# Optimization experiments

Hardware: AMD Instinct MI355X
Metric: run time of the kernel (lower is better)

## Reference

```python
import jax, jax.numpy as jnp
import numpy as np

# Model dims (match init_kwargs)
B, S, D, H = 2, 1024, 1024, 8
NKV = 1024            # num_key_values = nearest square to 4*D/4 = D -> 32^2
NK = 32               # sqrt(num_key_values) = PK num_keys
NP = 2                # product_keys
DK = D // 16          # PK dim_key
TK = 8                # product_key_topk == final_topk == key_value_pk_topk


def setup_inputs() -> dict:
    key = jax.random.key(0)
    ks = jax.random.split(key, 7)
    std = jnp.float32(0.02)
    return {
        "inputs": jax.random.normal(ks[0], (B, S, D), jnp.float32),
        "Wq": jax.random.normal(ks[1], (D * H, D), jnp.float32) * std,       # to_queries (torch Linear [out,in])
        "Wpk": jax.random.normal(ks[2], (DK * NP * H, D), jnp.float32) * std, # PK.to_queries
        "pk_keys": jax.random.normal(ks[3], (NP, NK, H, DK), jnp.float32) * std,
        "keys_emb": jax.random.normal(ks[4], (NKV * H, D), jnp.float32) * std,
        "values_emb": jax.random.normal(ks[5], (NKV * H, D), jnp.float32) * std,
        "Wo": jax.random.normal(ks[6], (D, D * H), jnp.float32) * std,        # to_out
    }


def reference(inputs, Wq, Wpk, pk_keys, keys_emb, values_emb, Wo):
    b, s, d = inputs.shape
    # queries: per-head dim == d; scale by d**-0.5
    q = (inputs @ Wq.T).reshape(b, s, H, d).transpose(0, 2, 1, 3) * (d ** -0.5)  # [B,H,S,D]

    # ---- PK product-key routing ----
    pq = (inputs @ Wpk.T).reshape(b, s, NP, H, DK)
    sim = jnp.einsum('bsphd,pnhd->pbshn', pq, pk_keys)          # [NP,B,S,H,NK]
    sc, ix = jax.lax.top_k(sim, TK)                             # [NP,B,S,H,TK]
    # combine the two sub-key spaces (strides = [1, NK])
    comb_ix = (ix[0][..., :, None] + ix[1][..., None, :] * NK).reshape(b, s, H, TK * TK)
    comb_sc = (sc[0][..., :, None] + sc[1][..., None, :]).reshape(b, s, H, TK * TK)
    fsc, pki = jax.lax.top_k(comb_sc, TK)                       # final_topk = TK
    fidx = jnp.take_along_axis(comb_ix, pki, axis=-1)           # [B,S,H,TK]
    w = jax.nn.softmax(fsc, axis=-1)                            # softmax_scores=True

    # ---- per-head offset + EmbeddingBag('sum') lookups with per-sample weights ----
    idx = fidx + (jnp.arange(H) * NKV)[None, None, :, None]     # [B,S,H,TK]
    k = jnp.einsum('bshtd,bsht->bhsd', keys_emb[idx], w)        # weighted-sum bag
    v = jnp.einsum('bshtd,bsht->bhsd', values_emb[idx], w)

    # ---- causal attention ----
    att = jnp.einsum('bhqd,bhkd->bhqk', q, k)                   # [B,H,S,S]
    causal = jnp.triu(jnp.ones((s, s), bool), 1)
    att = jnp.where(causal, -jnp.finfo(att.dtype).max, att)
    att = jax.nn.softmax(att, axis=-1)
    out = jnp.einsum('bhqk,bhkd->bqhd', att, v).reshape(b, s, H * d)
    return out @ Wo.T
```

## Files before the change

### kernel.cpp

```cpp
#include <hip/hip_runtime.h>
#include <hip/hip_bf16.h>

#define BB   2
#define SS   1024
#define DD   1024
#define HH   8
#define NPP  2
#define NKK  32
#define DKK  64
#define TKK  8
#define NKV_ 1024

typedef __hip_bfloat16 bf16;
typedef __attribute__((ext_vector_type(8))) short bf16x8;
typedef __attribute__((ext_vector_type(4))) float f32x4;

using u32g = __attribute__((address_space(1))) unsigned int;
using u32l = __attribute__((address_space(3))) unsigned int;

#define GLDS16(g, l) __builtin_amdgcn_global_load_lds((const u32g*)(g), (u32l*)(l), 16, 0, 0)

__device__ inline unsigned short f2b(float f) {
    unsigned x = __float_as_uint(f);
    return (unsigned short)((x + 0x7fffu + ((x >> 16) & 1u)) >> 16);
}
__device__ inline float b2f(unsigned short u) {
    return __uint_as_float(((unsigned)u) << 16);
}

__global__ __launch_bounds__(256) void cvt_bf(const float* __restrict__ src,
                                              bf16* __restrict__ dst, long long n)
{
    long long i = ((long long)blockIdx.x * 256 + threadIdx.x) * 4;
    if (i >= n) return;
    float4 v = *(const float4*)&src[i];
    ushort4 u; u.x = f2b(v.x); u.y = f2b(v.y); u.z = f2b(v.z); u.w = f2b(v.w);
    *(ushort4*)&dst[i] = u;
}

__global__ __launch_bounds__(256) void cvt_bf3(
    const float* __restrict__ s0, bf16* __restrict__ d0, long long n0,
    const float* __restrict__ s1, bf16* __restrict__ d1, long long n1,
    const float* __restrict__ s2, bf16* __restrict__ d2, long long n2)
{
    long long i = ((long long)blockIdx.x * 256 + threadIdx.x) * 4;
    const float* s; bf16* d;
    if (i < n0)                { s = s0 + i;            d = d0 + i; }
    else if (i < n0 + n1)      { s = s1 + (i - n0);     d = d1 + (i - n0); }
    else if (i < n0 + n1 + n2) { s = s2 + (i - n0 - n1); d = d2 + (i - n0 - n1); }
    else return;
    float4 v = *(const float4*)s;
    ushort4 u; u.x = f2b(v.x); u.y = f2b(v.y); u.z = f2b(v.z); u.w = f2b(v.w);
    *(ushort4*)d = u;
}

__global__ __launch_bounds__(256) void reduce_split(
    const float* __restrict__ p, float* __restrict__ out,
    long long n, int nsplit, float scale)
{
    long long i = ((long long)blockIdx.x * 256 + threadIdx.x) * 4;
    if (i >= n) return;
    float4 a = *(const float4*)&p[i];
    for (int s = 1; s < nsplit; ++s) {
        float4 b = *(const float4*)&p[i + (long long)s * n];
        a.x += b.x; a.y += b.y; a.z += b.z; a.w += b.w;
    }
    a.x *= scale; a.y *= scale; a.z *= scale; a.w *= scale;
    *(float4*)&out[i] = a;
}

template<typename TC, int CAUSAL, int GROUP>
__global__ __launch_bounds__(256) void mgemm(
    const bf16* __restrict__ A, const bf16* __restrict__ B, TC* __restrict__ C,
    int K, int lda, int ldb, int ldc,
    long long sAb, long long sAh, long long sBb, long long sBh,
    long long sCb, long long sCh, int zH, float scale)
{
    int gx = gridDim.x, gy = gridDim.y;
    int nwg = gx * gy * gridDim.z;
    int hw  = (blockIdx.z * gy + blockIdx.y) * gx + blockIdx.x;
    int w   = (hw & 7) * (nwg >> 3) + (hw >> 3);
    int z  = w / (gx * gy);
    int r  = w % (gx * gy);
    int bx = (r / (gy * GROUP)) * GROUP + (r % GROUP);
    int by = (r / GROUP) % gy;

    int zb = z / zH, zh = z % zH;
    A += (long long)zb * sAb + (long long)zh * sAh;
    B += (long long)zb * sBb + (long long)zh * sBh;
    C += (long long)zb * sCb + (long long)zh * sCh;

    int row0 = by * 128, col0 = bx * 128;
    if (CAUSAL == 1 && col0 > row0 + 127) return;
    int Klim = (CAUSAL == 2) ? min(K, row0 + 128) : K;

    __shared__ short sh[16384];
    short* As = sh;
    short* Bs = sh + 8192;

    int tid = threadIdx.x, wave = tid >> 6, lane = tid & 63;
    int wr = wave >> 1, wc = wave & 1;
    int lr = lane & 15, lg = lane >> 4;

    f32x4 zero = {0.f, 0.f, 0.f, 0.f};
    f32x4 acc[4][4];
    #pragma unroll
    for (int m = 0; m < 4; ++m)
        #pragma unroll
        for (int n = 0; n < 4; ++n) acc[m][n] = zero;

    int srow = wave * 32 + (lane >> 3);
    int scol = ((lane & 7) ^ (lane >> 3)) * 8;
    int fo = (lg ^ (lr & 7)) * 8;

    for (int k0 = 0; k0 < Klim; k0 += 64) {
        const bf16* Ak = A + (long long)(row0 + srow) * lda + k0 + scol;
        const bf16* Bk = B + (long long)(col0 + srow) * ldb + k0 + scol;
        #pragma unroll
        for (int i = 0; i < 4; ++i) {
            GLDS16(Ak + (long long)i * 8 * lda, &As[(wave * 32 + i * 8) * 64]);
            GLDS16(Bk + (long long)i * 8 * ldb, &Bs[(wave * 32 + i * 8) * 64]);
        }
        asm volatile("s_waitcnt vmcnt(0)" ::: "memory");
        __syncthreads();

        #pragma unroll
        for (int kk = 0; kk < 2; ++kk) {
            bf16x8 af[4], bfr[4];
            #pragma unroll
            for (int m = 0; m < 4; ++m)
                af[m] = *(const bf16x8*)&As[(wr * 64 + m * 16 + lr) * 64 + (fo ^ (kk * 32))];
            #pragma unroll
            for (int n = 0; n < 4; ++n)
                bfr[n] = *(const bf16x8*)&Bs[(wc * 64 + n * 16 + lr) * 64 + (fo ^ (kk * 32))];
            #pragma unroll
            for (int m = 0; m < 4; ++m)
                #pragma unroll
                for (int n = 0; n < 4; ++n)
                    acc[m][n] = __builtin_amdgcn_mfma_f32_16x16x32_bf16(
                        bfr[n], af[m], acc[m][n], 0, 0, 0);
        }
        __syncthreads();
    }

    #pragma unroll
    for (int m = 0; m < 4; ++m) {
        long long row = row0 + wr * 64 + m * 16 + lr;
        #pragma unroll
        for (int n = 0; n < 4; ++n) {
            int col = col0 + wc * 64 + n * 16 + lg * 4;
            if constexpr (sizeof(TC) == 2) {
                ushort4 o;
                o.x = f2b(scale * acc[m][n][0]);
                o.y = f2b(scale * acc[m][n][1]);
                o.z = f2b(scale * acc[m][n][2]);
                o.w = f2b(scale * acc[m][n][3]);
                *(ushort4*)&C[row * ldc + col] = o;
            } else {
                *(float4*)&C[row * ldc + col] = make_float4(
                    scale * acc[m][n][0], scale * acc[m][n][1],
                    scale * acc[m][n][2], scale * acc[m][n][3]);
            }
        }
    }
}

#define TILE 64
#define KT   16
#define LPAD 4
__global__ __launch_bounds__(256) void pq_fix(
    const float* __restrict__ A, const float* __restrict__ Bm, float* __restrict__ P)
{
    long long zo = (long long)blockIdx.z * 1024 * 1024;
    A += zo;
    int col0 = blockIdx.x * TILE;
    int kbase = blockIdx.y * 256;
    __shared__ float As[KT][TILE + LPAD];
    __shared__ float Bs[KT][TILE + LPAD];
    int tid = threadIdx.x, tx = tid % 16, ty = tid / 16;
    float acc[4][4] = {{0.f}};
    int lr = tid / 4, lk = (tid % 4) * 4;

    for (int k0 = kbase; k0 < kbase + 256; k0 += KT) {
        float4 va = *(const float4*)&A[(long long)lr * 1024 + k0 + lk];
        As[lk + 0][lr] = va.x; As[lk + 1][lr] = va.y;
        As[lk + 2][lr] = va.z; As[lk + 3][lr] = va.w;
        float4 vb = *(const float4*)&Bm[(long long)(col0 + lr) * 1024 + k0 + lk];
        Bs[lk + 0][lr] = vb.x; Bs[lk + 1][lr] = vb.y;
        Bs[lk + 2][lr] = vb.z; Bs[lk + 3][lr] = vb.w;
        __syncthreads();
        #pragma unroll
        for (int kk = 0; kk < KT; ++kk) {
            float a[4], b[4];
            #pragma unroll
            for (int i = 0; i < 4; ++i) a[i] = As[kk][ty * 4 + i];
            #pragma unroll
            for (int j = 0; j < 4; ++j) b[j] = Bs[kk][tx * 4 + j];
            #pragma unroll
            for (int i = 0; i < 4; ++i)
                #pragma unroll
                for (int j = 0; j < 4; ++j)
                    acc[i][j] = fmaf(a[i], b[j], acc[i][j]);
        }
        __syncthreads();
    }
    long long base = ((long long)(blockIdx.y * 2 + blockIdx.z) * 64) * 1024;
    #pragma unroll
    for (int i = 0; i < 4; ++i)
        *(float4*)&P[base + (long long)(ty * 4 + i) * 1024 + col0 + tx * 4] =
            make_float4(acc[i][0], acc[i][1], acc[i][2], acc[i][3]);
}

__global__ __launch_bounds__(256) void pq_fix_red(
    const float* __restrict__ P, float* __restrict__ pqb)
{
    long long i4 = ((long long)blockIdx.x * 256 + threadIdx.x) * 4;
    if (i4 >= 131072) return;
    float4 a = *(const float4*)&P[i4];
    #pragma unroll
    for (int sp = 1; sp < 4; ++sp) {
        float4 b = *(const float4*)&P[(long long)sp * 131072 + i4];
        a.x += b.x; a.y += b.y; a.z += b.z; a.w += b.w;
    }
    long long z = i4 >> 16, rem = i4 & 65535;
    *(float4*)&pqb[z * 1048576 + rem] = a;
}

__device__ inline unsigned ord_f32(float f) {
    unsigned u = __float_as_uint(f);
    return (u >> 31) ? ~u : (u | 0x80000000u);
}
__device__ inline float unord_f32(unsigned m) {
    unsigned u = (m >> 31) ? (m ^ 0x80000000u) : ~m;
    return __uint_as_float(u);
}

__global__ __launch_bounds__(256) void pk_route(
    const float* __restrict__ pq, const float* __restrict__ pkk,
    float* __restrict__ wts, int* __restrict__ idxs)
{
    int bid  = blockIdx.x * 4 + (threadIdx.x >> 6);
    int lane = threadIdx.x & 63;
    int h    = bid % HH;
    long long bs = bid / HH;
    int p = lane >> 5, n = lane & 31;

    const float* pv = pq  + (bs * NPP + p) * (HH * DKK) + h * DKK;
    const float* kv = pkk + ((long long)(p * NKK + n) * HH + h) * DKK;
    float s = 0.f;
    #pragma unroll
    for (int d = 0; d < DKK; d += 4) {
        float4 q4 = *(const float4*)&pv[d];
        float4 k4 = *(const float4*)&kv[d];
        s = fmaf(q4.x, k4.x, fmaf(q4.y, k4.y, fmaf(q4.z, k4.z, fmaf(q4.w, k4.w, s))));
    }

    unsigned long long key =
        ((unsigned long long)ord_f32(s) << 32) | (unsigned)(31 - n);
    #pragma unroll
    for (int k = 2; k <= 32; k <<= 1) {
        #pragma unroll
        for (int j = k >> 1; j > 0; j >>= 1) {
            unsigned long long other = __shfl_xor(key, j);
            bool keep_big = ((n & k) == 0) == ((n & j) == 0);
            key = (keep_big == (other > key)) ? other : key;
        }
    }
    float keepv = unord_f32((unsigned)(key >> 32));
    int   keepn = 31 - (int)(key & 31);

    int ci = lane >> 3, cj = lane & 7;
    float c0 = __shfl(keepv, ci);
    float c1 = __shfl(keepv, 32 + cj);
    float cv = c0 + c1;

    unsigned long long k2 =
        ((unsigned long long)ord_f32(cv) << 32) | (unsigned)(63 - lane);
    #pragma unroll
    for (int k = 2; k <= 64; k <<= 1) {
        #pragma unroll
        for (int j = k >> 1; j > 0; j >>= 1) {
            unsigned long long other = __shfl_xor(k2, j);
            bool keep_big = ((lane & k) == 0) == ((lane & j) == 0);
            k2 = (keep_big == (other > k2)) ? other : k2;
        }
    }
    int   f   = 63 - (int)(k2 & 63);
    float fsv = unord_f32((unsigned)(k2 >> 32));
    int n0 = __shfl(keepn, f >> 3);
    int n1 = __shfl(keepn, 32 + (f & 7));
    int fsi = n0 + n1 * NKK;

    float m0 = __shfl(fsv, 0);
    float e = (lane < TKK) ? expf(fsv - m0) : 0.f;
    float sum = e;
    #pragma unroll
    for (int off = 1; off < 8; off <<= 1) sum += __shfl_xor(sum, off);
    if (lane < TKK) {
        wts[(long long)bid * TKK + lane]  = e / sum;
        idxs[(long long)bid * TKK + lane] = fsi + h * NKV_;
    }
}

__global__ __launch_bounds__(256) void gather_kv(
    const bf16* __restrict__ keb, const bf16* __restrict__ veb,
    const float* __restrict__ wts, const int* __restrict__ idxs,
    bf16* __restrict__ kb, bf16* __restrict__ vsd)
{
    int bid = blockIdx.x;
    int h = bid % HH;
    int bs = bid / HH;
    int b = bs / SS, s = bs % SS;

    float w[TKK]; long long rb[TKK];
    #pragma unroll
    for (int t = 0; t < TKK; ++t) {
        w[t]  = wts[(long long)bid * TKK + t];
        rb[t] = (long long)idxs[(long long)bid * TKK + t] * DD;
    }
    int c0 = threadIdx.x * 4;
    long long off = (((long long)b * HH + h) * SS + s) * DD + c0;

    ushort4 ld[TKK];
    #pragma unroll
    for (int t = 0; t < TKK; ++t) ld[t] = *(const ushort4*)&keb[rb[t] + c0];
    float4 a = {0.f, 0.f, 0.f, 0.f};
    #pragma unroll
    for (int t = 0; t < TKK; ++t) {
        a.x += w[t] * b2f(ld[t].x); a.y += w[t] * b2f(ld[t].y);
        a.z += w[t] * b2f(ld[t].z); a.w += w[t] * b2f(ld[t].w);
    }
    ushort4 o; o.x = f2b(a.x); o.y = f2b(a.y); o.z = f2b(a.z); o.w = f2b(a.w);
    *(ushort4*)&kb[off] = o;

    #pragma unroll
    for (int t = 0; t < TKK; ++t) ld[t] = *(const ushort4*)&veb[rb[t] + c0];
    a = make_float4(0.f, 0.f, 0.f, 0.f);
    #pragma unroll
    for (int t = 0; t < TKK; ++t) {
        a.x += w[t] * b2f(ld[t].x); a.y += w[t] * b2f(ld[t].y);
        a.z += w[t] * b2f(ld[t].z); a.w += w[t] * b2f(ld[t].w);
    }
    o.x = f2b(a.x); o.y = f2b(a.y); o.z = f2b(a.z); o.w = f2b(a.w);
    *(ushort4*)&vsd[off] = o;
}

__global__ __launch_bounds__(256) void tr64ip(bf16* __restrict__ m)
{
    __shared__ unsigned short La[64][65];
    __shared__ unsigned short Lb[64][65];
    unsigned short* M = (unsigned short*)m + (long long)blockIdx.y * SS * DD;

    int p = blockIdx.x, ti = 0;
    while (p >= 16 - ti) { p -= 16 - ti; ++ti; }
    int tj = ti + p;
    int a0r = ti * 64, a0c = tj * 64;
    int b0r = tj * 64, b0c = ti * 64;

    int r = threadIdx.x / 16, c4 = (threadIdx.x % 16) * 4;
    #pragma unroll
    for (int i = 0; i < 4; ++i) {
        int sr = r + i * 16;
        ushort4 va = *(const ushort4*)&M[(long long)(a0r + sr) * DD + a0c + c4];
        La[sr][c4] = va.x; La[sr][c4+1] = va.y; La[sr][c4+2] = va.z; La[sr][c4+3] = va.w;
        if (ti != tj) {
            ushort4 vb = *(const ushort4*)&M[(long long)(b0r + sr) * DD + b0c + c4];
            Lb[sr][c4] = vb.x; Lb[sr][c4+1] = vb.y; Lb[sr][c4+2] = vb.z; Lb[sr][c4+3] = vb.w;
        }
    }
    __syncthreads();
    #pragma unroll
    for (int i = 0; i < 4; ++i) {
        int dr = r + i * 16;
        ushort4 va;
        va.x = La[c4][dr]; va.y = La[c4+1][dr]; va.z = La[c4+2][dr]; va.w = La[c4+3][dr];
        *(ushort4*)&M[(long long)(b0r + dr) * DD + b0c + c4] = va;
        if (ti != tj) {
            ushort4 vb;
            vb.x = Lb[c4][dr]; vb.y = Lb[c4+1][dr]; vb.z = Lb[c4+2][dr]; vb.w = Lb[c4+3][dr];
            *(ushort4*)&M[(long long)(a0r + dr) * DD + a0c + c4] = vb;
        }
    }
}

__global__ __launch_bounds__(256) void softmax_rows(bf16* __restrict__ sc)
{
    int r    = blockIdx.x * 4 + (threadIdx.x >> 6);
    int lane = threadIdx.x & 63;
    int sq   = r % SS;
    unsigned short* row = (unsigned short*)(sc + (long long)r * SS);
    int nvalid = sq + 1;
    int wlim = ((sq >> 7) + 1) << 7;
    int base = lane * 16;

    uint4 u0 = *(const uint4*)&row[base];
    uint4 u1 = *(const uint4*)&row[base + 8];
    unsigned uw[8] = {u0.x, u0.y, u0.z, u0.w, u1.x, u1.y, u1.z, u1.w};

    float v[16];
    float m = -INFINITY;
    #pragma unroll
    for (int i = 0; i < 8; ++i) {
        int j0 = base + i * 2;
        v[i*2]   = (j0     < nvalid) ? __uint_as_float(uw[i] << 16)          : -INFINITY;
        v[i*2+1] = (j0 + 1 < nvalid) ? __uint_as_float(uw[i] & 0xffff0000u) : -INFINITY;
        m = fmaxf(m, fmaxf(v[i*2], v[i*2+1]));
    }
    #pragma unroll
    for (int off = 1; off < 64; off <<= 1) m = fmaxf(m, __shfl_xor(m, off));

    float e[16], ls = 0.f;
    #pragma unroll
    for (int i = 0; i < 16; ++i) {
        e[i] = (base + i < nvalid) ? expf(v[i] - m) : 0.f;
        ls += e[i];
    }
    #pragma unroll
    for (int off = 1; off < 64; off <<= 1) ls += __shfl_xor(ls, off);
    float inv = 1.f / ls;

    if (base < wlim) {
        unsigned ow[8];
        #pragma unroll
        for (int i = 0; i < 8; ++i)
            ow[i] = (unsigned)f2b(e[i*2] * inv) | ((unsigned)f2b(e[i*2+1] * inv) << 16);
        *(uint4*)&row[base]     = make_uint4(ow[0], ow[1], ow[2], ow[3]);
        *(uint4*)&row[base + 8] = make_uint4(ow[4], ow[5], ow[6], ow[7]);
    }
}

extern "C" void kernel_launch(void* const* d_in, const int* in_sizes, int n_in,
                              void* d_out, int out_size, void* d_ws, size_t ws_size,
                              hipStream_t stream)
{
    const float* inputs     = (const float*)d_in[0];
    const float* Wq         = (const float*)d_in[1];
    const float* Wpk        = (const float*)d_in[2];
    const float* pk_keys    = (const float*)d_in[3];
    const float* keys_emb   = (const float*)d_in[4];
    const float* values_emb = (const float*)d_in[5];
    const float* Wo         = (const float*)d_in[6];
    float* out = (float*)d_out;

    const long long MB = 1LL << 20;
    char* base = (char*)d_ws;
    bf16* kb  = (bf16*)(base);
    float* spl = (float*)base;
    bf16* qc  = (bf16*)(base + 32*MB);
    bf16* vt  = (bf16*)(base + 64*MB);
    char* screg = base + 96*MB;
    bf16* scb = (bf16*)screg;
    float* pqb = (float*)screg;
    bf16* Wpkb = (bf16*)(screg + 8*MB);
    bf16* Wqb  = (bf16*)(screg + 10*MB);
    bf16* xb   = (bf16*)(screg + 26*MB);
    bf16* keb  = (bf16*)screg;
    bf16* veb  = (bf16*)(screg + 16*MB);
    bf16* Wob  = (bf16*)screg;
    float* wtb = (float*)(base + 128*MB);
    int*   ixb = (int*)(base + 128*MB + (512<<10));
    size_t needed = (size_t)(129*MB);
    if (ws_size < needed) return;

    const long long SLAB = (long long)SS * HH * DD;
    const long long SD   = (long long)SS * DD;
    const long long OUTN = 2048LL * 1024;

    cvt_bf3<<<dim3(11264), 256, 0, stream>>>(
        inputs, xb, 2097152LL, Wpk, Wpkb, 1048576LL, Wq, Wqb, 8388608LL);

    mgemm<float, 0, 1><<<dim3(8, 16, 2), 256, 0, stream>>>(
        xb, Wpkb, spl, 512, 1024, 1024, 1024,
        512, 0, 512, 0, OUTN, 0, 1, 1.0f);
    reduce_split<<<dim3(2048), 256, 0, stream>>>(spl, pqb, OUTN, 2, 1.0f);

    pq_fix<<<dim3(16, 4, 2), 256, 0, stream>>>(inputs, Wpk, spl);
    pq_fix_red<<<dim3(128), 256, 0, stream>>>(spl, pqb);

    pk_route<<<dim3(BB * SS * HH / 4), 256, 0, stream>>>(pqb, pk_keys, wtb, ixb);

    mgemm<bf16, 0, 8><<<dim3(64, 16, 1), 256, 0, stream>>>(
        xb, Wqb, qc, 1024, 1024, 1024, 8192,
        0, 0, 0, 0, 0, 0, 1, 0.03125f);

    cvt_bf3<<<dim3(16384), 256, 0, stream>>>(
        keys_emb, keb, 8388608LL, values_emb, veb, 8388608LL,
        (const float*)nullptr, (bf16*)nullptr, 0LL);

    gather_kv<<<dim3(BB * SS * HH), 256, 0, stream>>>(
        keb, veb, wtb, ixb, kb, vt);

    tr64ip<<<dim3(136, BB * HH), 256, 0, stream>>>(vt);

    mgemm<bf16, 1, 1><<<dim3(8, 8, BB * HH), 256, 0, stream>>>(
        qc, kb, scb, 1024, 8192, 1024, 1024,
        SLAB, (long long)DD, (long long)HH * SD, SD,
        (long long)HH * SS * SS, (long long)SS * SS, HH, 1.0f);

    softmax_rows<<<dim3(BB * HH * SS / 4), 256, 0, stream>>>(scb);

    mgemm<bf16, 2, 1><<<dim3(8, 8, BB * HH), 256, 0, stream>>>(
        scb, vt, qc, 1024, 1024, 1024, 8192,
        (long long)HH * SS * SS, (long long)SS * SS,
        (long long)HH * SD, SD,
        SLAB, (long long)DD, HH, 1.0f);

    cvt_bf<<<dim3(8192), 256, 0, stream>>>(Wo, Wob, 8388608LL);

    mgemm<float, 0, 1><<<dim3(8, 16, 4), 256, 0, stream>>>(
        qc, Wob, spl, 2048, 8192, 8192, 1024,
        2048, 0, 2048, 0, OUTN, 0, 1, 1.0f);
    reduce_split<<<dim3(2048), 256, 0, stream>>>(spl, out, OUTN, 4, 1.0f);
}
```

Before: 356.9 us.

## Pipeline GEMM K-loop with four-stage LDS ring buffer

```diff
diff --git a/kernel.cpp b/kernel.cpp
--- a/kernel.cpp
+++ b/kernel.cpp
@@ -93,10 +93,9 @@
     int row0 = by * 128, col0 = bx * 128;
     if (CAUSAL == 1 && col0 > row0 + 127) return;
     int Klim = (CAUSAL == 2) ? min(K, row0 + 128) : K;
-
-    __shared__ short sh[16384];
-    short* As = sh;
-    short* Bs = sh + 8192;
+    int nt = Klim >> 6;
+
+    __shared__ short sh[4][16384];
 
     int tid = threadIdx.x, wave = tid >> 6, lane = tid & 63;
     int wr = wave >> 1, wc = wave & 1;
@@ -113,17 +112,35 @@
     int scol = ((lane & 7) ^ (lane >> 3)) * 8;
     int fo = (lg ^ (lr & 7)) * 8;
 
-    for (int k0 = 0; k0 < Klim; k0 += 64) {
-        const bf16* Ak = A + (long long)(row0 + srow) * lda + k0 + scol;
-        const bf16* Bk = B + (long long)(col0 + srow) * ldb + k0 + scol;
+    const bf16* Abase = A + (long long)(row0 + srow) * lda + scol;
+    const bf16* Bbase = B + (long long)(col0 + srow) * ldb + scol;
+
+    auto STAGE = [&](int b, int t) {
+        int k0 = t * 64;
+        short* As = &sh[b][0];
+        short* Bs = &sh[b][8192];
         #pragma unroll
         for (int i = 0; i < 4; ++i) {
-            GLDS16(Ak + (long long)i * 8 * lda, &As[(wave * 32 + i * 8) * 64]);
-            GLDS16(Bk + (long long)i * 8 * ldb, &Bs[(wave * 32 + i * 8) * 64]);
-        }
-        asm volatile("s_waitcnt vmcnt(0)" ::: "memory");
-        __syncthreads();
-
+            GLDS16(Abase + (long long)i * 8 * lda + k0, &As[(wave * 32 + i * 8) * 64]);
+            GLDS16(Bbase + (long long)i * 8 * ldb + k0, &Bs[(wave * 32 + i * 8) * 64]);
+        }
+    };
+
+    STAGE(0, 0);
+    if (nt > 1) STAGE(1, 1);
+    if (nt > 2) STAGE(2, 2);
+
+    for (int t = 0; t < nt; ++t) {
+        if (t + 3 < nt) STAGE((t + 3) & 3, t + 3);
+        int rem = nt - 1 - t;
+        if (rem >= 3)      asm volatile("s_waitcnt vmcnt(24)" ::: "memory");
+        else if (rem == 2) asm volatile("s_waitcnt vmcnt(16)" ::: "memory");
+        else if (rem == 1) asm volatile("s_waitcnt vmcnt(8)"  ::: "memory");
+        else               asm volatile("s_waitcnt vmcnt(0)"  ::: "memory");
+        __builtin_amdgcn_s_barrier();
+
+        const short* As = &sh[t & 3][0];
+        const short* Bs = &sh[t & 3][8192];
         #pragma unroll
         for (int kk = 0; kk < 2; ++kk) {
             bf16x8 af[4], bfr[4];
@@ -140,7 +157,9 @@
                     acc[m][n] = __builtin_amdgcn_mfma_f32_16x16x32_bf16(
                         bfr[n], af[m], acc[m][n], 0, 0, 0);
         }
-        __syncthreads();
+
+        asm volatile("s_waitcnt lgkmcnt(0)" ::: "memory");
+        __builtin_amdgcn_s_barrier();
     }
 
     #pragma unroll
```

Result: slower. 402.8 us (+12.9%).

## Fuse PK query projection into Q projection GEMM and prune combined top-k candidates

Applied to the files above, without the earlier changes.

```diff
diff --git a/kernel.cpp b/kernel.cpp
--- a/kernel.cpp
+++ b/kernel.cpp
@@ -69,12 +69,13 @@
     *(float4*)&out[i] = a;
 }
 
-template<typename TC, int CAUSAL, int GROUP>
+template<typename TC, int CAUSAL, int GROUP, int MODE>
 __global__ __launch_bounds__(256) void mgemm(
     const bf16* __restrict__ A, const bf16* __restrict__ B, TC* __restrict__ C,
     int K, int lda, int ldb, int ldc,
     long long sAb, long long sAh, long long sBb, long long sBh,
-    long long sCb, long long sCh, int zH, float scale)
+    long long sCb, long long sCh, int zH, float scale,
+    float* __restrict__ C2)
 {
     int gx = gridDim.x, gy = gridDim.y;
     int nwg = gx * gy * gridDim.z;
@@ -143,6 +144,21 @@
         __syncthreads();
     }
 
+    if constexpr (MODE == 1) {
+        if (col0 >= 8192) {
+            #pragma unroll
+            for (int m = 0; m < 4; ++m) {
+                long long row = row0 + wr * 64 + m * 16 + lr;
+                #pragma unroll
+                for (int n = 0; n < 4; ++n) {
+                    int col = col0 - 8192 + wc * 64 + n * 16 + lg * 4;
+                    *(float4*)&C2[row * 1024 + col] = make_float4(
+                        acc[m][n][0], acc[m][n][1], acc[m][n][2], acc[m][n][3]);
+                }
+            }
+            return;
+        }
+    }
     #pragma unroll
     for (int m = 0; m < 4; ++m) {
         long long row = row0 + wr * 64 + m * 16 + lr;
@@ -269,19 +285,27 @@
     float keepv = unord_f32((unsigned)(key >> 32));
     int   keepn = 31 - (int)(key & 31);
 
-    int ci = lane >> 3, cj = lane & 7;
-    float c0 = __shfl(keepv, ci);
-    float c1 = __shfl(keepv, 32 + cj);
+    int l5 = lane & 31;
+    int ii, jj;
+    if (l5 < 8)       { ii = 0;       jj = l5; }
+    else if (l5 < 12) { ii = 1;       jj = l5 - 8; }
+    else if (l5 < 14) { ii = 2;       jj = l5 - 12; }
+    else if (l5 < 16) { ii = 3;       jj = l5 - 14; }
+    else              { ii = l5 - 12; jj = 0; }
+    float c0 = __shfl(keepv, ii);
+    float c1 = __shfl(keepv, 32 + jj);
     float cv = c0 + c1;
-
-    unsigned long long k2 =
-        ((unsigned long long)ord_f32(cv) << 32) | (unsigned)(63 - lane);
-    #pragma unroll
-    for (int k = 2; k <= 64; k <<= 1) {
+    int fcell = ii * 8 + jj;
+
+    unsigned long long k2 = (l5 < 20)
+        ? (((unsigned long long)ord_f32(cv) << 32) | (unsigned)(63 - fcell))
+        : 0ull;
+    #pragma unroll
+    for (int k = 2; k <= 32; k <<= 1) {
         #pragma unroll
         for (int j = k >> 1; j > 0; j >>= 1) {
             unsigned long long other = __shfl_xor(k2, j);
-            bool keep_big = ((lane & k) == 0) == ((lane & j) == 0);
+            bool keep_big = ((l5 & k) == 0) == ((l5 & j) == 0);
             k2 = (keep_big == (other > k2)) ? other : k2;
         }
     }
@@ -446,13 +470,14 @@
     char* base = (char*)d_ws;
     bf16* kb  = (bf16*)(base);
     float* spl = (float*)base;
+    float* spl2 = (float*)(base + 16*MB);
     bf16* qc  = (bf16*)(base + 32*MB);
     bf16* vt  = (bf16*)(base + 64*MB);
     char* screg = base + 96*MB;
     bf16* scb = (bf16*)screg;
     float* pqb = (float*)screg;
-    bf16* Wpkb = (bf16*)(screg + 8*MB);
-    bf16* Wqb  = (bf16*)(screg + 10*MB);
+    bf16* Wqb  = (bf16*)(screg + 8*MB);
+    bf16* Wpkb = (bf16*)(screg + 24*MB);
     bf16* xb   = (bf16*)(screg + 26*MB);
     bf16* keb  = (bf16*)screg;
     bf16* veb  = (bf16*)(screg + 16*MB);
@@ -467,21 +492,17 @@
     const long long OUTN = 2048LL * 1024;
 
     cvt_bf3<<<dim3(11264), 256, 0, stream>>>(
-        inputs, xb, 2097152LL, Wpk, Wpkb, 1048576LL, Wq, Wqb, 8388608LL);
-
-    mgemm<float, 0, 1><<<dim3(8, 16, 2), 256, 0, stream>>>(
-        xb, Wpkb, spl, 512, 1024, 1024, 1024,
-        512, 0, 512, 0, OUTN, 0, 1, 1.0f);
-    reduce_split<<<dim3(2048), 256, 0, stream>>>(spl, pqb, OUTN, 2, 1.0f);
-
-    pq_fix<<<dim3(16, 4, 2), 256, 0, stream>>>(inputs, Wpk, spl);
-    pq_fix_red<<<dim3(128), 256, 0, stream>>>(spl, pqb);
+        inputs, xb, 2097152LL, Wq, Wqb, 8388608LL, Wpk, Wpkb, 1048576LL);
+
+    pq_fix<<<dim3(16, 4, 2), 256, 0, stream>>>(inputs, Wpk, spl2);
+
+    mgemm<bf16, 0, 8, 1><<<dim3(72, 16, 1), 256, 0, stream>>>(
+        xb, Wqb, qc, 1024, 1024, 1024, 8192,
+        0, 0, 0, 0, 0, 0, 1, 0.03125f, pqb);
+
+    pq_fix_red<<<dim3(128), 256, 0, stream>>>(spl2, pqb);
 
     pk_route<<<dim3(BB * SS * HH / 4), 256, 0, stream>>>(pqb, pk_keys, wtb, ixb);
-
-    mgemm<bf16, 0, 8><<<dim3(64, 16, 1), 256, 0, stream>>>(
-        xb, Wqb, qc, 1024, 1024, 1024, 8192,
-        0, 0, 0, 0, 0, 0, 1, 0.03125f);
 
     cvt_bf3<<<dim3(16384), 256, 0, stream>>>(
         keys_emb, keb, 8388608LL, values_emb, veb, 8388608LL,
@@ -492,23 +513,23 @@
 
     tr64ip<<<dim3(136, BB * HH), 256, 0, stream>>>(vt);
 
-    mgemm<bf16, 1, 1><<<dim3(8, 8, BB * HH), 256, 0, stream>>>(
+    mgemm<bf16, 1, 1, 0><<<dim3(8, 8, BB * HH), 256, 0, stream>>>(
         qc, kb, scb, 1024, 8192, 1024, 1024,
         SLAB, (long long)DD, (long long)HH * SD, SD,
-        (long long)HH * SS * SS, (long long)SS * SS, HH, 1.0f);
+        (long long)HH * SS * SS, (long long)SS * SS, HH, 1.0f, nullptr);
 
     softmax_rows<<<dim3(BB * HH * SS / 4), 256, 0, stream>>>(scb);
 
-    mgemm<bf16, 2, 1><<<dim3(8, 8, BB * HH), 256, 0, stream>>>(
+    mgemm<bf16, 2, 1, 0><<<dim3(8, 8, BB * HH), 256, 0, stream>>>(
         scb, vt, qc, 1024, 1024, 1024, 8192,
         (long long)HH * SS * SS, (long long)SS * SS,
         (long long)HH * SD, SD,
-        SLAB, (long long)DD, HH, 1.0f);
+        SLAB, (long long)DD, HH, 1.0f, nullptr);
 
     cvt_bf<<<dim3(8192), 256, 0, stream>>>(Wo, Wob, 8388608LL);
 
-    mgemm<float, 0, 1><<<dim3(8, 16, 4), 256, 0, stream>>>(
+    mgemm<float, 0, 1, 0><<<dim3(8, 16, 4), 256, 0, stream>>>(
         qc, Wob, spl, 2048, 8192, 8192, 1024,
-        2048, 0, 2048, 0, OUTN, 0, 1, 1.0f);
+        2048, 0, 2048, 0, OUTN, 0, 1, 1.0f, nullptr);
     reduce_split<<<dim3(2048), 256, 0, stream>>>(spl, out, OUTN, 4, 1.0f);
 }
```

After: 345.1 us, median of 2. 1.03x faster.
